# Optimization experiments

Measured on AMD Instinct MI355X. Metric: run time of the kernel, lower is better.

The kernel has to match this reference:

```python
import jax, jax.numpy as jnp
import numpy as np

N_NODES = 100000
N_EDGES = 3200000
IN_DIM = 128
OUT_DIM = 128


def setup_inputs() -> dict:
    key = jax.random.key(0)
    k1, k2, k3, k4, k5 = jax.random.split(key, 5)
    features = jax.random.normal(k1, (N_NODES, IN_DIM), dtype=jnp.float32)
    edge_src = jax.random.randint(k2, (N_EDGES,), 0, N_NODES, dtype=jnp.int32)
    edge_dst = jax.random.randint(k3, (N_EDGES,), 0, N_NODES, dtype=jnp.int32)
    edge_vals = jax.random.uniform(k4, (N_EDGES,), dtype=jnp.float32)
    # kaiming_normal_ on [in, out] with fan_in = in
    weight = jax.random.normal(k5, (IN_DIM, OUT_DIM), dtype=jnp.float32) * np.sqrt(2.0 / IN_DIM)
    bias = jnp.zeros((OUT_DIM,), dtype=jnp.float32)
    return {
        "features": features,
        "edge_src": edge_src,
        "edge_dst": edge_dst,
        "edge_vals": edge_vals,
        "weight": weight,
        "bias": bias,
    }


def reference(features, edge_src, edge_dst, edge_vals, weight, bias):
    # h = X @ W  : [N, out]
    h = features @ weight
    # SpMM: out[dst] += A[dst, src] * h[src]   (COO edge-list aggregation)
    msgs = h[edge_src] * edge_vals[:, None]          # [E, out]
    agg = jax.ops.segment_sum(msgs, edge_dst, num_segments=N_NODES)
    return agg + bias
```

## Files before the change

### kernel.cpp

```cpp
#include <hip/hip_runtime.h>

#define IN_DIM 128
#define OUT_DIM 128
#define BIN_SHIFT 9
#define BIN_NODES 512
#define CAP1 18432
#define TILE_A 3072

typedef __attribute__((ext_vector_type(8))) short bf16x8;
typedef __attribute__((ext_vector_type(4))) float f32x4;
typedef __attribute__((ext_vector_type(2))) float f32x2;

__device__ inline unsigned short f2bf(float f) {
    unsigned u = __float_as_uint(f);
    unsigned r = (u + 0x7fff + ((u >> 16) & 1)) >> 16;
    return (unsigned short)r;
}
__device__ inline float bflo(unsigned h) { return __uint_as_float(h << 16); }
__device__ inline float bfhi(unsigned h) { return __uint_as_float(h & 0xffff0000u); }

__global__ __launch_bounds__(256) void pack_w_zero(const float* __restrict__ W,
                                                   unsigned short* __restrict__ Wpack,
                                                   int* __restrict__ gcur, int nbin) {
    int idx = blockIdx.x * 256 + threadIdx.x;
    if (blockIdx.x == 0 && threadIdx.x < nbin) gcur[threadIdx.x] = 0;
    if (idx >= 16384) return;
    int j = idx & 7;
    int lane = (idx >> 3) & 63;
    int kc = (idx >> 9) & 3;
    int tn = idx >> 11;
    int k = kc * 32 + (lane >> 4) * 8 + j;
    int n = tn * 16 + (lane & 15);
    Wpack[idx] = f2bf(W[k * OUT_DIM + n]);
}

struct BinSmem {
    int2 eL[TILE_A];
    int hist[256];
    int dbase[256];
    unsigned char bL[TILE_A];
};

__global__ __launch_bounds__(256) void phase1(
    const int* __restrict__ src, const int* __restrict__ dst,
    const float* __restrict__ vals, int* __restrict__ gcur,
    int2* __restrict__ entries, int n_edges, int nbin, int nA,
    const float* __restrict__ X, const unsigned short* __restrict__ Wpack,
    unsigned short* __restrict__ Hb, int n_rows, int nG) {
    __shared__ BinSmem sm;

    int b = blockIdx.x;
    int isGemm, widx;
    if (b < 2 * nG) {
        isGemm = (b & 1) == 0;
        widx = b >> 1;
    } else {
        isGemm = 0;
        widx = nG + (b - 2 * nG);
    }

    const int tid = threadIdx.x;

    if (!isGemm) {
        const int base = widx * TILE_A;
        const int n = min(TILE_A, n_edges - base);

        for (int i = tid; i < nbin; i += 256) sm.hist[i] = 0;
        __syncthreads();

        for (int i = tid; i < n; i += 256) {
            int d = dst[base + i];
            int s = src[base + i];
            float v = vals[base + i];
            int bin = d >> BIN_SHIFT;
            sm.eL[i] = make_int2(s | ((d & (BIN_NODES - 1)) << 17), __float_as_int(v));
            sm.bL[i] = (unsigned char)bin;
            atomicAdd(&sm.hist[bin], 1);
        }
        __syncthreads();

        for (int l = tid; l < nbin; l += 256) {
            int c = sm.hist[l];
            sm.dbase[l] = (c > 0) ? atomicAdd(&gcur[l], c) : 0;
            sm.hist[l] = 0;
        }
        __syncthreads();

        for (int i = tid; i < n; i += 256) {
            int bin = sm.bL[i];
            int pos = sm.dbase[bin] + atomicAdd(&sm.hist[bin], 1);
            if (pos < CAP1) entries[(long long)bin * CAP1 + pos] = sm.eL[i];
        }
        return;
    }

    int strip = widx * 4 + (tid >> 6);
    long long m0 = (long long)strip * 32;
    if (m0 >= n_rows) return;
    int lane = tid & 63;
    int quad = lane >> 4;
    int low = lane & 15;

    const bf16x8* B = (const bf16x8*)Wpack;

    long long r0 = m0 + low;
    long long r1 = m0 + 16 + low;
    if (r1 >= n_rows) r1 = n_rows - 1;
    if (r0 >= n_rows) r0 = n_rows - 1;

    f32x4 acc[2][8] = {};

#pragma unroll
    for (int kc = 0; kc < 4; ++kc) {
        const float4* p0 = (const float4*)(X + r0 * IN_DIM + kc * 32 + quad * 8);
        const float4* p1 = (const float4*)(X + r1 * IN_DIM + kc * 32 + quad * 8);
        float4 x0a = p0[0], x0b = p0[1];
        float4 x1a = p1[0], x1b = p1[1];
        bf16x8 afr0, afr1;
        afr0[0] = f2bf(x0a.x); afr0[1] = f2bf(x0a.y); afr0[2] = f2bf(x0a.z); afr0[3] = f2bf(x0a.w);
        afr0[4] = f2bf(x0b.x); afr0[5] = f2bf(x0b.y); afr0[6] = f2bf(x0b.z); afr0[7] = f2bf(x0b.w);
        afr1[0] = f2bf(x1a.x); afr1[1] = f2bf(x1a.y); afr1[2] = f2bf(x1a.z); afr1[3] = f2bf(x1a.w);
        afr1[4] = f2bf(x1b.x); afr1[5] = f2bf(x1b.y); afr1[6] = f2bf(x1b.z); afr1[7] = f2bf(x1b.w);
#pragma unroll
        for (int tn = 0; tn < 8; ++tn) {
            bf16x8 bfr = B[(tn * 4 + kc) * 64 + lane];
            acc[0][tn] = __builtin_amdgcn_mfma_f32_16x16x32_bf16(afr0, bfr, acc[0][tn], 0, 0, 0);
            acc[1][tn] = __builtin_amdgcn_mfma_f32_16x16x32_bf16(afr1, bfr, acc[1][tn], 0, 0, 0);
        }
    }

#pragma unroll
    for (int t = 0; t < 2; ++t) {
#pragma unroll
        for (int tn = 0; tn < 8; ++tn) {
#pragma unroll
            for (int r = 0; r < 4; ++r) {
                long long row = m0 + t * 16 + quad * 4 + r;
                if (row < n_rows) {
                    int col = tn * 16 + low;
                    Hb[row * OUT_DIM + col] = f2bf(acc[t][tn][r]);
                }
            }
        }
    }
}

__global__ __launch_bounds__(1024) void binB(const int2* __restrict__ entries,
                                             const int* __restrict__ gcur,
                                             int2* __restrict__ csr,
                                             int2* __restrict__ node_meta,
                                             int n_nodes) {
    __shared__ int hist[BIN_NODES];
    __shared__ int off[BIN_NODES];

    const int bin = blockIdx.x;
    const int tid = threadIdx.x;
    const int cnt = min(gcur[bin], CAP1);
    const long long base = (long long)bin * CAP1;

    for (int i = tid; i < BIN_NODES; i += 1024) hist[i] = 0;
    __syncthreads();

    for (int i = tid; i < cnt; i += 1024) {
        int l = (entries[base + i].x >> 17) & (BIN_NODES - 1);
        atomicAdd(&hist[l], 1);
    }
    __syncthreads();

    if (tid < BIN_NODES) off[tid] = hist[tid];
    __syncthreads();
    for (int d = 1; d < BIN_NODES; d <<= 1) {
        int v = 0;
        if (tid < BIN_NODES && tid >= d) v = off[tid - d];
        __syncthreads();
        if (tid < BIN_NODES) off[tid] += v;
        __syncthreads();
    }
    if (tid < BIN_NODES) {
        int ex = off[tid] - hist[tid];
        int node = bin * BIN_NODES + tid;
        if (node < n_nodes) node_meta[node] = make_int2((int)(base + ex), hist[tid]);
        off[tid] = ex;
    }
    __syncthreads();

    for (int i = tid; i < cnt; i += 1024) {
        int2 e = entries[base + i];
        int l = (e.x >> 17) & (BIN_NODES - 1);
        int pos = atomicAdd(&off[l], 1);
        csr[base + pos] = e;
    }
}

__global__ __launch_bounds__(256) void gather_nodes(
    const int2* __restrict__ node_meta, const int2* __restrict__ csr,
    const unsigned short* __restrict__ Hb, const float* __restrict__ bias,
    float* __restrict__ out, int n_nodes) {
    int node = blockIdx.x * 4 + (threadIdx.x >> 6);
    if (node >= n_nodes) return;
    int lane = threadIdx.x & 63;

    int2 meta = node_meta[node];
    int beg = meta.x;
    int end = meta.x + meta.y;

    f32x2 acc;
    {
        float2 bb = ((const float2*)bias)[lane];
        acc[0] = bb.x; acc[1] = bb.y;
    }

    int e = beg;
    for (; e + 8 <= end; e += 8) {
        int2 c[8];
#pragma unroll
        for (int j = 0; j < 8; ++j) c[j] = csr[e + j];
        unsigned h[8];
#pragma unroll
        for (int j = 0; j < 8; ++j)
            h[j] = *(const unsigned*)(Hb + (long long)(c[j].x & 0x1ffff) * OUT_DIM + lane * 2);
#pragma unroll
        for (int j = 0; j < 8; ++j) {
            float v = __int_as_float(c[j].y);
            f32x2 hv; hv[0] = bflo(h[j]); hv[1] = bfhi(h[j]);
            f32x2 vv; vv[0] = v; vv[1] = v;
            acc += vv * hv;
        }
    }
    for (; e < end; ++e) {
        int2 c0 = csr[e];
        unsigned h0 = *(const unsigned*)(Hb + (long long)(c0.x & 0x1ffff) * OUT_DIM + lane * 2);
        float v = __int_as_float(c0.y);
        f32x2 hv; hv[0] = bflo(h0); hv[1] = bfhi(h0);
        f32x2 vv; vv[0] = v; vv[1] = v;
        acc += vv * hv;
    }

    float2 res; res.x = acc[0]; res.y = acc[1];
    ((float2*)(out + (long long)node * OUT_DIM))[lane] = res;
}

extern "C" void kernel_launch(void* const* d_in, const int* in_sizes, int n_in,
                              void* d_out, int out_size, void* d_ws, size_t ws_size,
                              hipStream_t stream) {
    const float* features  = (const float*)d_in[0];
    const int* edge_src    = (const int*)d_in[1];
    const int* edge_dst    = (const int*)d_in[2];
    const float* edge_vals = (const float*)d_in[3];
    const float* weight    = (const float*)d_in[4];
    const float* bias      = (const float*)d_in[5];

    const int n_nodes = in_sizes[0] / IN_DIM;
    const int n_edges = in_sizes[1];
    const int nbin = (n_nodes + BIN_NODES - 1) / BIN_NODES;

    int2* entries       = (int2*)d_ws;
    int2* csr           = entries + (long long)nbin * CAP1;
    int2* node_meta     = csr + (long long)nbin * CAP1;
    unsigned short* Hb  = (unsigned short*)(node_meta + n_nodes);
    unsigned short* Wp  = Hb + (long long)n_nodes * OUT_DIM;
    int* gcur           = (int*)(Wp + 16384);

    float* out = (float*)d_out;

    pack_w_zero<<<64, 256, 0, stream>>>(weight, Wp, gcur, nbin);

    const int nA = (n_edges + TILE_A - 1) / TILE_A;
    const int n_strips = (n_nodes + 31) / 32;
    const int nG = (n_strips + 3) / 4;
    phase1<<<nA + nG, 256, 0, stream>>>(edge_src, edge_dst, edge_vals, gcur,
                                        entries, n_edges, nbin, nA,
                                        features, Wp, Hb, n_nodes, nG);

    binB<<<nbin, 1024, 0, stream>>>(entries, gcur, csr, node_meta, n_nodes);

    gather_nodes<<<(n_nodes + 3) / 4, 256, 0, stream>>>(
        node_meta, csr, Hb, bias, out, n_nodes);
}
```

Measured before the change: 322.9 us.

## Co-schedule the X@W GEMM with per-bin CSR build instead of edge binning

The dense X@W GEMM blocks move out of the first binning kernel, where they were interleaved with the edge-scatter blocks, and into the second-stage kernel. That kernel now alternates bin-local CSR construction blocks with GEMM blocks at 1024 threads, so each GEMM block covers 16 strips. Edge binning becomes its own standalone kernel. The goal is to hide the GEMM behind the low-parallelism, sync-heavy per-bin counting sort rather than have it compete with the bandwidth-bound scatter. In exchange, the GEMM now runs at 1024-thread granularity, and the grid size depends on nbin matching the number of GEMM groups.

```diff
diff --git a/kernel.cpp b/kernel.cpp
--- a/kernel.cpp
+++ b/kernel.cpp
@@ -41,60 +41,99 @@
     unsigned char bL[TILE_A];
 };
 
-__global__ __launch_bounds__(256) void phase1(
+__global__ __launch_bounds__(256) void binA(
     const int* __restrict__ src, const int* __restrict__ dst,
     const float* __restrict__ vals, int* __restrict__ gcur,
-    int2* __restrict__ entries, int n_edges, int nbin, int nA,
+    int2* __restrict__ entries, int n_edges, int nbin) {
+    __shared__ BinSmem sm;
+
+    const int tid = threadIdx.x;
+    const int base = blockIdx.x * TILE_A;
+    const int n0 = n_edges - base;
+    if (n0 <= 0) return;
+    const int n = (n0 < TILE_A) ? n0 : TILE_A;
+
+    for (int i = tid; i < nbin; i += 256) sm.hist[i] = 0;
+    __syncthreads();
+
+    for (int i = tid; i < n; i += 256) {
+        int d = dst[base + i];
+        int s = src[base + i];
+        float v = vals[base + i];
+        int bin = d >> BIN_SHIFT;
+        sm.eL[i] = make_int2(s | ((d & (BIN_NODES - 1)) << 17), __float_as_int(v));
+        sm.bL[i] = (unsigned char)bin;
+        atomicAdd(&sm.hist[bin], 1);
+    }
+    __syncthreads();
+
+    for (int l = tid; l < nbin; l += 256) {
+        int c = sm.hist[l];
+        sm.dbase[l] = (c > 0) ? atomicAdd(&gcur[l], c) : 0;
+        sm.hist[l] = 0;
+    }
+    __syncthreads();
+
+    for (int i = tid; i < n; i += 256) {
+        int bin = sm.bL[i];
+        int pos = sm.dbase[bin] + atomicAdd(&sm.hist[bin], 1);
+        if (pos < CAP1) entries[(long long)bin * CAP1 + pos] = sm.eL[i];
+    }
+}
+
+__global__ __launch_bounds__(1024) void gemm_binB(
+    const int2* __restrict__ entries, const int* __restrict__ gcur,
+    int2* __restrict__ csr, int2* __restrict__ node_meta, int n_nodes,
     const float* __restrict__ X, const unsigned short* __restrict__ Wpack,
-    unsigned short* __restrict__ Hb, int n_rows, int nG) {
-    __shared__ BinSmem sm;
-
-    int b = blockIdx.x;
-    int isGemm, widx;
-    if (b < 2 * nG) {
-        isGemm = (b & 1) == 0;
-        widx = b >> 1;
-    } else {
-        isGemm = 0;
-        widx = nG + (b - 2 * nG);
-    }
-
+    unsigned short* __restrict__ Hb, int n_rows) {
+    __shared__ int hist[BIN_NODES];
+    __shared__ int off[BIN_NODES];
+
+    const int b = blockIdx.x;
+    const int widx = b >> 1;
     const int tid = threadIdx.x;
 
-    if (!isGemm) {
-        const int base = widx * TILE_A;
-        const int n = min(TILE_A, n_edges - base);
-
-        for (int i = tid; i < nbin; i += 256) sm.hist[i] = 0;
-        __syncthreads();
-
-        for (int i = tid; i < n; i += 256) {
-            int d = dst[base + i];
-            int s = src[base + i];
-            float v = vals[base + i];
-            int bin = d >> BIN_SHIFT;
-            sm.eL[i] = make_int2(s | ((d & (BIN_NODES - 1)) << 17), __float_as_int(v));
-            sm.bL[i] = (unsigned char)bin;
-            atomicAdd(&sm.hist[bin], 1);
-        }
-        __syncthreads();
-
-        for (int l = tid; l < nbin; l += 256) {
-            int c = sm.hist[l];
-            sm.dbase[l] = (c > 0) ? atomicAdd(&gcur[l], c) : 0;
-            sm.hist[l] = 0;
-        }
-        __syncthreads();
-
-        for (int i = tid; i < n; i += 256) {
-            int bin = sm.bL[i];
-            int pos = sm.dbase[bin] + atomicAdd(&sm.hist[bin], 1);
-            if (pos < CAP1) entries[(long long)bin * CAP1 + pos] = sm.eL[i];
+    if ((b & 1) == 0) {
+        const int bin = widx;
+        const int cnt = min(gcur[bin], CAP1);
+        const long long base = (long long)bin * CAP1;
+
+        for (int i = tid; i < BIN_NODES; i += 1024) hist[i] = 0;
+        __syncthreads();
+
+        for (int i = tid; i < cnt; i += 1024) {
+            int l = (entries[base + i].x >> 17) & (BIN_NODES - 1);
+            atomicAdd(&hist[l], 1);
+        }
+        __syncthreads();
+
+        if (tid < BIN_NODES) off[tid] = hist[tid];
+        __syncthreads();
+        for (int d = 1; d < BIN_NODES; d <<= 1) {
+            int v = 0;
+            if (tid < BIN_NODES && tid >= d) v = off[tid - d];
+            __syncthreads();
+            if (tid < BIN_NODES) off[tid] += v;
+            __syncthreads();
+        }
+        if (tid < BIN_NODES) {
+            int ex = off[tid] - hist[tid];
+            int node = bin * BIN_NODES + tid;
+            if (node < n_nodes) node_meta[node] = make_int2((int)(base + ex), hist[tid]);
+            off[tid] = ex;
+        }
+        __syncthreads();
+
+        for (int i = tid; i < cnt; i += 1024) {
+            int2 e = entries[base + i];
+            int l = (e.x >> 17) & (BIN_NODES - 1);
+            int pos = atomicAdd(&off[l], 1);
+            csr[base + pos] = e;
         }
         return;
     }
 
-    int strip = widx * 4 + (tid >> 6);
+    int strip = widx * 16 + (tid >> 6);
     long long m0 = (long long)strip * 32;
     if (m0 >= n_rows) return;
     int lane = tid & 63;
@@ -145,53 +184,6 @@
     }
 }
 
-__global__ __launch_bounds__(1024) void binB(const int2* __restrict__ entries,
-                                             const int* __restrict__ gcur,
-                                             int2* __restrict__ csr,
-                                             int2* __restrict__ node_meta,
-                                             int n_nodes) {
-    __shared__ int hist[BIN_NODES];
-    __shared__ int off[BIN_NODES];
-
-    const int bin = blockIdx.x;
-    const int tid = threadIdx.x;
-    const int cnt = min(gcur[bin], CAP1);
-    const long long base = (long long)bin * CAP1;
-
-    for (int i = tid; i < BIN_NODES; i += 1024) hist[i] = 0;
-    __syncthreads();
-
-    for (int i = tid; i < cnt; i += 1024) {
-        int l = (entries[base + i].x >> 17) & (BIN_NODES - 1);
-        atomicAdd(&hist[l], 1);
-    }
-    __syncthreads();
-
-    if (tid < BIN_NODES) off[tid] = hist[tid];
-    __syncthreads();
-    for (int d = 1; d < BIN_NODES; d <<= 1) {
-        int v = 0;
-        if (tid < BIN_NODES && tid >= d) v = off[tid - d];
-        __syncthreads();
-        if (tid < BIN_NODES) off[tid] += v;
-        __syncthreads();
-    }
-    if (tid < BIN_NODES) {
-        int ex = off[tid] - hist[tid];
-        int node = bin * BIN_NODES + tid;
-        if (node < n_nodes) node_meta[node] = make_int2((int)(base + ex), hist[tid]);
-        off[tid] = ex;
-    }
-    __syncthreads();
-
-    for (int i = tid; i < cnt; i += 1024) {
-        int2 e = entries[base + i];
-        int l = (e.x >> 17) & (BIN_NODES - 1);
-        int pos = atomicAdd(&off[l], 1);
-        csr[base + pos] = e;
-    }
-}
-
 __global__ __launch_bounds__(256) void gather_nodes(
     const int2* __restrict__ node_meta, const int2* __restrict__ csr,
     const unsigned short* __restrict__ Hb, const float* __restrict__ bias,
@@ -266,13 +258,14 @@
     pack_w_zero<<<64, 256, 0, stream>>>(weight, Wp, gcur, nbin);
 
     const int nA = (n_edges + TILE_A - 1) / TILE_A;
+    binA<<<nA, 256, 0, stream>>>(edge_src, edge_dst, edge_vals, gcur,
+                                 entries, n_edges, nbin);
+
     const int n_strips = (n_nodes + 31) / 32;
-    const int nG = (n_strips + 3) / 4;
-    phase1<<<nA + nG, 256, 0, stream>>>(edge_src, edge_dst, edge_vals, gcur,
-                                        entries, n_edges, nbin, nA,
-                                        features, Wp, Hb, n_nodes, nG);
-
-    binB<<<nbin, 1024, 0, stream>>>(entries, gcur, csr, node_meta, n_nodes);
+    const int nGg = (n_strips + 15) / 16;
+    gemm_binB<<<2 * ((nbin > nGg) ? nbin : nGg), 1024, 0, stream>>>(
+        entries, gcur, csr, node_meta, n_nodes,
+        features, Wp, Hb, n_nodes);
 
     gather_nodes<<<(n_nodes + 3) / 4, 256, 0, stream>>>(
         node_meta, csr, Hb, bias, out, n_nodes);
```

Result: no change. 323.5 us (+0.2%).
